# Kernel tuning notes

Hardware: AMD Instinct MI355X
Metric: run time of the kernel (lower is better)

Reference implementation:

```python
import jax, jax.numpy as jnp
import numpy as np

C, T, H = 256, 16, 8
D = C // H  # head dim = 32
SCALE = float((D * T) ** 0.5)


def setup_inputs() -> dict:
    key = jax.random.key(0)
    kx, kk, kq, kv = jax.random.split(key, 4)
    B, P = 8, 1024
    x = jax.random.normal(kx, (B, C, P, T), dtype=jnp.float32)
    # 1x1 conv weights, no bias -> [out_ch, in_ch]
    Wk = jax.random.normal(kk, (C, C), dtype=jnp.float32) * 0.02
    Wq = jax.random.normal(kq, (C, C), dtype=jnp.float32) * 0.02
    Wv = jax.random.normal(kv, (C, C), dtype=jnp.float32) * 0.02
    return {"x": x, "Wk": Wk, "Wq": Wq, "Wv": Wv}


def _proj_split(W, x):
    # 1x1 conv == channel matmul, then split heads: b (h d) p t -> b h d p t
    B, _, P, Tt = x.shape
    y = jnp.einsum('oc,bcpt->bopt', W, x)
    return y.reshape(B, H, D, P, Tt)


def reference(x, Wk, Wq, Wv):
    B, _, P, Tt = x.shape
    k = _proj_split(Wk, x)  # [B,H,D,P,T]
    q = _proj_split(Wq, x)
    v = _proj_split(Wv, x)
    # energy over spatial positions, contracting head-dim and time
    energy = jnp.einsum('bhdpt,bhdqt->bhpq', k, q)  # [B,H,P,P]
    attn = jax.nn.softmax(energy / SCALE, axis=-1)
    out = jnp.einsum('bhpq,bhdpt->bhdqt', attn, v)  # [B,H,D,P,T]
    return out.reshape(B, C, P, Tt)
```

## Files before the change

### kernel.cpp

```cpp
#include <hip/hip_runtime.h>


typedef unsigned short u16;
typedef unsigned int u32;
typedef unsigned long long u64;
typedef __attribute__((ext_vector_type(8))) short bfx8;
typedef __attribute__((ext_vector_type(4))) float fx4;

constexpr float KC1 = 1.4426950408889634f / 22.627416997969522f;

__device__ __forceinline__ u16 f2bf(float f) {
  u32 u = __builtin_bit_cast(u32, f);
  return (u16)((u + 0x7fffu + ((u >> 16) & 1u)) >> 16);
}
__device__ __forceinline__ float bf2f(u16 v) {
  return __builtin_bit_cast(float, (u32)v << 16);
}
__device__ __forceinline__ fx4 mfma16(bfx8 a, bfx8 b, fx4 c) {
  return __builtin_amdgcn_mfma_f32_16x16x32_bf16(a, b, c, 0, 0, 0);
}
typedef __attribute__((address_space(1))) const unsigned int* as1p;
typedef __attribute__((address_space(3))) unsigned int* as3p;
__device__ __forceinline__ void gll16(const void* g, void* l) {
  __builtin_amdgcn_global_load_lds((as1p)g, (as3p)l, 16, 0, 0);
}
#define SB0 __builtin_amdgcn_sched_barrier(0)

template <bool SWAP, int NT, int LK>
__device__ __forceinline__ void gemm1g(const u16* __restrict__ Ag,
                                       const u16* __restrict__ Bg,
                                       u16* lds, fx4 (&acc)[2][4][2][2],
                                       int wv, int lane) {
  const int l15 = lane & 15, kg = lane >> 4, l7 = lane & 7;
  const int wr = wv >> 2, wn = wv & 3;
  const int rsub = lane >> 3, csub = (lane & 7) * 8;
  constexpr int A0 = 0, A1 = 16384, B0 = 32768, B1 = 49152;
  bfx8 af[2][4][2];
  bfx8 bf[2][2][2];

  auto stg = [&](const u16* g, int ldsoff, int tile, int half) {
    const u16* gp = g + (size_t)(half * 128 + wv * 16 + rsub) * LK + tile * 64 + csub;
    u16* lp = lds + ldsoff + half * 8192 + wv * 1024;
    gll16(gp, lp);
    gll16(gp + (size_t)8 * LK, lp + 512);
  };
  auto stgA = [&](int t, int buf) {
    int aoff = buf ? A1 : A0;
    stg(Ag, aoff, t, 0); stg(Ag, aoff, t, 1);
  };
  auto stgB = [&](int t, int buf) {
    int boff = buf ? B1 : B0;
    stg(Bg, boff, t, 0); stg(Bg, boff, t, 1);
  };
  auto LA = [&](int boff, int mh) {
    const u16* base = lds + boff + mh * 8192 + wr * 4096;
#pragma unroll
    for (int mt = 0; mt < 4; ++mt)
#pragma unroll
      for (int kk = 0; kk < 2; ++kk)
        af[mh][mt][kk] = *(const bfx8*)(base + (mt * 16 + l15) * 64 + (((kk << 2) + kg) ^ l7) * 8);
  };
  auto LB = [&](int boff, int nh) {
    const u16* base = lds + boff + nh * 8192 + wn * 2048;
#pragma unroll
    for (int nt = 0; nt < 2; ++nt)
#pragma unroll
      for (int kk = 0; kk < 2; ++kk)
        bf[nh][nt][kk] = *(const bfx8*)(base + (nt * 16 + l15) * 64 + (((kk << 2) + kg) ^ l7) * 8);
  };
  auto MM = [&](int mh, int nh) {
    __builtin_amdgcn_s_setprio(1);
#pragma unroll
    for (int mt = 0; mt < 4; ++mt)
#pragma unroll
      for (int nt = 0; nt < 2; ++nt)
#pragma unroll
        for (int kk = 0; kk < 2; ++kk)
          if constexpr (SWAP)
            acc[mh][mt][nh][nt] = mfma16(bf[nh][nt][kk], af[mh][mt][kk], acc[mh][mt][nh][nt]);
          else
            acc[mh][mt][nh][nt] = mfma16(af[mh][mt][kk], bf[nh][nt][kk], acc[mh][mt][nh][nt]);
    __builtin_amdgcn_s_setprio(0);
  };

  stgA(0, 0); stgB(0, 0);
  stgA(1, 1); stgB(1, 1);
  asm volatile("s_waitcnt vmcnt(8)" ::: "memory");
  __builtin_amdgcn_s_barrier();
  SB0;
  LA(A0, 0);
  LB(B0, 0);

#pragma unroll 1
  for (int t = 0; t < NT - 1; ++t) {
    const int cur = t & 1, nxt = cur ^ 1;
    const int cA = cur ? A1 : A0, cB = cur ? B1 : B0;
    const int nA = cur ? A0 : A1, nB = cur ? B0 : B1;
    LA(cA, 1);
    MM(0, 0);
    LB(cB, 1);
    MM(1, 0);
    asm volatile("s_waitcnt lgkmcnt(0)" ::: "memory");
    asm volatile("s_waitcnt vmcnt(0)" ::: "memory");
    __builtin_amdgcn_s_barrier();
    SB0;
    LB(nB, 0);
    if (t + 2 < NT) stgA(t + 2, cur);
    MM(0, 1);
    LA(nA, 0);
    if (t + 2 < NT) stgB(t + 2, cur);
    MM(1, 1);
  }
  {
    constexpr int cur = (NT - 1) & 1;
    constexpr int cA = cur ? A1 : A0, cB = cur ? B1 : B0;
    LA(cA, 1);
    MM(0, 0);
    LB(cB, 1);
    MM(1, 0);
    MM(0, 1);
    MM(1, 1);
  }
}

__global__ __launch_bounds__(256) void k_wconv(const float* __restrict__ Wk,
                                               const float* __restrict__ Wq,
                                               const float* __restrict__ Wv,
                                               u16* __restrict__ Wall) {
  int blk = blockIdx.x;
  int pr = blk >> 5;
  const float* src = (pr == 0) ? Wk : ((pr == 1) ? Wq : Wv);
  int oc = (blk & 31) * 8 + (threadIdx.x >> 5);
  int Cc = threadIdx.x & 31;
  const float4* s4 = (const float4*)(src + oc * 256 + Cc * 8);
  float4 a = s4[0], b = s4[1];
  alignas(16) u16 t[8] = {f2bf(a.x), f2bf(a.y), f2bf(a.z), f2bf(a.w),
                          f2bf(b.x), f2bf(b.y), f2bf(b.z), f2bf(b.w)};
  int o = pr * 256 + oc;
  int pos = (Cc & ~7) + ((Cc & 7) ^ (o & 7));
  *(uint4*)(Wall + o * 256 + pos * 8) = *(const uint4*)t;
}

__global__ __launch_bounds__(256) void k_xt(const float* __restrict__ x,
                                            u16* __restrict__ Xbf) {
  __shared__ u16 Xs[128 * 256];
  int b = blockIdx.x >> 7;
  int n0 = (blockIdx.x & 127) * 128;
  int tid = threadIdx.x;
  int ng = tid & 31, cgrp = tid >> 5;
  const float* xb = x + (size_t)b * 4194304 + n0 + ng * 4;
#pragma unroll
  for (int it = 0; it < 4; ++it) {
    int Cc = cgrp + it * 8;
    float4 v[8];
#pragma unroll
    for (int i = 0; i < 8; ++i)
      v[i] = *(const float4*)(xb + (size_t)(Cc * 8 + i) * 16384);
#pragma unroll
    for (int j = 0; j < 4; ++j) {
      int n = ng * 4 + j;
      alignas(16) u16 c8v[8];
#pragma unroll
      for (int i = 0; i < 8; ++i) c8v[i] = f2bf(((const float*)&v[i])[j]);
      int pos = (Cc & ~7) + ((Cc & 7) ^ (n & 7));
      *(uint4*)&Xs[n * 256 + pos * 8] = *(const uint4*)c8v;
    }
  }
  __syncthreads();
  u16* xo = Xbf + (size_t)b * 4194304 + (size_t)n0 * 256;
#pragma unroll
  for (int it = 0; it < 16; ++it) {
    int idx = tid + it * 256;
    int n = idx >> 5, chp = idx & 31;
    uint4 v = *(const uint4*)&Xs[n * 256 + chp * 8];
    *(uint4*)&xo[(size_t)n * 256 + chp * 8] = v;
  }
}

__global__ __launch_bounds__(512) void k_proj2(const u16* __restrict__ Xbf,
                                               const u16* __restrict__ Wall,
                                               u16* __restrict__ Kb, u16* __restrict__ Qb,
                                               u16* __restrict__ Vb) {
  __shared__ u16 lds[65536];
  int bid = blockIdx.x;
  int vid = (bid & 7) * 192 + (bid >> 3);
  int nidx = vid / 3;
  int otile = vid - nidx * 3;
  int b = nidx >> 6, ntile = nidx & 63;
  int tid = threadIdx.x, lane = tid & 63, wv = tid >> 6;
  int l15 = lane & 15, kg = lane >> 4;
  int wr = wv >> 2, wn = wv & 3;
  const u16* Ag = Wall + otile * 65536;
  const u16* Bg = Xbf + (size_t)b * 4194304 + (size_t)ntile * 65536;
  fx4 acc[2][4][2][2];
#pragma unroll
  for (int mh = 0; mh < 2; ++mh)
#pragma unroll
    for (int mt = 0; mt < 4; ++mt)
#pragma unroll
      for (int nh = 0; nh < 2; ++nh)
#pragma unroll
        for (int nt = 0; nt < 2; ++nt) acc[mh][mt][nh][nt] = (fx4)0.0f;

  gemm1g<false, 4, 256>(Ag, Bg, lds, acc, wv, lane);

  u16* dst = (otile == 0) ? Kb : ((otile == 1) ? Qb : Vb);
#pragma unroll
  for (int mh = 0; mh < 2; ++mh)
#pragma unroll
    for (int mt = 0; mt < 4; ++mt) {
      int o = mh * 128 + wr * 64 + mt * 16 + kg * 4;
      int h = o >> 5;
      size_t bhro = (size_t)(b * 8 + h) * 524288;
#pragma unroll
      for (int nh = 0; nh < 2; ++nh)
#pragma unroll
        for (int nt = 0; nt < 2; ++nt) {
          int p = ntile * 16 + nh * 8 + wn * 2 + nt;
          size_t ro = bhro + (size_t)p * 512;
          int p7 = p & 7;
#pragma unroll
          for (int j = 0; j < 4; ++j) {
            int f = ((o & 31) + j) * 16 + l15;
            int ch = (f >> 3) ^ p7;
            dst[ro + ch * 8 + (f & 7)] = f2bf(acc[mh][mt][nh][nt][j]);
          }
        }
    }
}

__global__ __launch_bounds__(512) void k_egemm(const u16* __restrict__ Qb,
                                               const u16* __restrict__ Kb,
                                               u16* __restrict__ Pt,
                                               float* __restrict__ Zpart) {
  __shared__ u16 lds[65536];
  int bid = blockIdx.x;
  int vid = (bid & 7) * 128 + (bid >> 3);
  int bh = vid >> 4, qt = (vid >> 2) & 3, pt = vid & 3;
  int q0 = qt * 256, p0 = pt * 256;
  int tid = threadIdx.x, lane = tid & 63, wv = tid >> 6;
  int l15 = lane & 15, kg = lane >> 4;
  int wr = wv >> 2, wn = wv & 3;
  const u16* Ag = Qb + (size_t)bh * 524288 + (size_t)q0 * 512;
  const u16* Bg = Kb + (size_t)bh * 524288 + (size_t)p0 * 512;
  fx4 acc[2][4][2][2];
#pragma unroll
  for (int mh = 0; mh < 2; ++mh)
#pragma unroll
    for (int mt = 0; mt < 4; ++mt)
#pragma unroll
      for (int nh = 0; nh < 2; ++nh)
#pragma unroll
        for (int nt = 0; nt < 2; ++nt) acc[mh][mt][nh][nt] = (fx4)0.0f;

  gemm1g<true, 8, 512>(Ag, Bg, lds, acc, wv, lane);

  size_t pbase = (size_t)bh * 1048576;
  float zac[2][2][4];
#pragma unroll
  for (int nh = 0; nh < 2; ++nh)
#pragma unroll
    for (int nt = 0; nt < 2; ++nt)
#pragma unroll
      for (int j = 0; j < 4; ++j) zac[nh][nt][j] = 0.f;
#pragma unroll
  for (int mh = 0; mh < 2; ++mh)
#pragma unroll
    for (int mt = 0; mt < 4; ++mt) {
      int q = q0 + mh * 128 + wr * 64 + mt * 16 + l15;
      size_t qrow = pbase + (size_t)q * 1024;
      int q7 = l15 & 7;
#pragma unroll
      for (int nh = 0; nh < 2; ++nh)
#pragma unroll
        for (int nt = 0; nt < 2; ++nt) {
          int p4 = p0 + nh * 128 + wn * 32 + nt * 16 + kg * 4;
          alignas(8) u16 e4[4];
#pragma unroll
          for (int j = 0; j < 4; ++j) {
            float e = exp2f(acc[mh][mt][nh][nt][j] * KC1);
            zac[nh][nt][j] += e;
            e4[j] = f2bf(e);
          }
          int ch = (p4 >> 3) ^ q7;
          *(u64*)(Pt + qrow + ch * 8 + (p4 & 7)) = *(const u64*)e4;
        }
    }
#pragma unroll
  for (int nh = 0; nh < 2; ++nh)
#pragma unroll
    for (int nt = 0; nt < 2; ++nt)
#pragma unroll
      for (int j = 0; j < 4; ++j) {
        float v = zac[nh][nt][j];
        v += __shfl_xor(v, 1);
        v += __shfl_xor(v, 2);
        v += __shfl_xor(v, 4);
        v += __shfl_xor(v, 8);
        zac[nh][nt][j] = v;
      }
  if (l15 == 0) {
    size_t zb = (size_t)(qt * 2 + wr) * 65536 + (size_t)bh * 1024;
#pragma unroll
    for (int nh = 0; nh < 2; ++nh)
#pragma unroll
      for (int nt = 0; nt < 2; ++nt) {
        int p4 = p0 + nh * 128 + wn * 32 + nt * 16 + kg * 4;
        float4 zv;
        zv.x = zac[nh][nt][0]; zv.y = zac[nh][nt][1];
        zv.z = zac[nh][nt][2]; zv.w = zac[nh][nt][3];
        *(float4*)&Zpart[zb + p4] = zv;
      }
  }
}

__global__ __launch_bounds__(256) void k_zfinal(const float* __restrict__ Zpart,
                                                float* __restrict__ RZ) {
  int idx = blockIdx.x * 256 + threadIdx.x;
  float s = 0.f;
#pragma unroll
  for (int k = 0; k < 8; ++k) s += Zpart[(size_t)k * 65536 + idx];
  RZ[idx] = 1.0f / s;
}

__global__ __launch_bounds__(256) void k_vt(const u16* __restrict__ Vb,
                                            const float* __restrict__ RZ,
                                            u16* __restrict__ Vt) {
  __shared__ u16 Vl[64 * 512];
  int bh = blockIdx.x >> 4;
  int ptile = blockIdx.x & 15;
  int tid = threadIdx.x;
  const u16* src = Vb + (size_t)bh * 524288 + (size_t)ptile * 32768;
#pragma unroll
  for (int it = 0; it < 16; ++it) {
    int idx = tid + it * 256;
    int pl = idx >> 6, g = idx & 63;
    float rz = RZ[bh * 1024 + ptile * 64 + pl];
    uint4 v = *(const uint4*)&src[(size_t)pl * 512 + g * 8];
    int cf = g ^ (pl & 7);
    u32 w[4] = {v.x, v.y, v.z, v.w};
    alignas(16) u16 c8v[8];
#pragma unroll
    for (int i = 0; i < 4; ++i) {
      c8v[2 * i]     = f2bf(bf2f((u16)w[i]) * rz);
      c8v[2 * i + 1] = f2bf(bf2f((u16)(w[i] >> 16)) * rz);
    }
    *(uint4*)&Vl[pl * 512 + cf * 8] = *(const uint4*)c8v;
  }
  __syncthreads();
  u16* dst = Vt + (size_t)bh * 524288;
#pragma unroll
  for (int it = 0; it < 16; ++it) {
    int f = (tid & 63) + (it & 7) * 64;
    int pc = (tid >> 6) * 2 + (it >> 3);
    int base = pc * 8 * 512 + f;
    u32 x0 = (u32)Vl[base] | ((u32)Vl[base + 512] << 16);
    u32 x1 = (u32)Vl[base + 1024] | ((u32)Vl[base + 1536] << 16);
    u32 x2 = (u32)Vl[base + 2048] | ((u32)Vl[base + 2560] << 16);
    u32 x3 = (u32)Vl[base + 3072] | ((u32)Vl[base + 3584] << 16);
    uint4 pk; pk.x = x0; pk.y = x1; pk.z = x2; pk.w = x3;
    int col = ptile * 8 + (pc ^ (f & 7));
    *(uint4*)&dst[(size_t)f * 1024 + col * 8] = pk;
  }
}

__global__ __launch_bounds__(512) void k_pv(const u16* __restrict__ Pt,
                                            const u16* __restrict__ Vt,
                                            float* __restrict__ out) {
  __shared__ u16 lds[65536];
  int bid = blockIdx.x;
  int vid = (bid & 7) * 64 + (bid >> 3);
  int bh = vid >> 3, tile = vid & 7;
  int q0 = (tile >> 1) * 256, f0 = (tile & 1) * 256;
  int tid = threadIdx.x, lane = tid & 63, wv = tid >> 6;
  int l15 = lane & 15, kg = lane >> 4;
  int wr = wv >> 2, wn = wv & 3;
  const u16* Ag = Pt + (size_t)bh * 1048576 + (size_t)q0 * 1024;
  const u16* Bg = Vt + (size_t)bh * 524288 + (size_t)f0 * 1024;
  fx4 acc[2][4][2][2];
#pragma unroll
  for (int mh = 0; mh < 2; ++mh)
#pragma unroll
    for (int mt = 0; mt < 4; ++mt)
#pragma unroll
      for (int nh = 0; nh < 2; ++nh)
#pragma unroll
        for (int nt = 0; nt < 2; ++nt) acc[mh][mt][nh][nt] = (fx4)0.0f;

  gemm1g<false, 16, 1024>(Ag, Bg, lds, acc, wv, lane);

#pragma unroll
  for (int mh = 0; mh < 2; ++mh)
#pragma unroll
    for (int mt = 0; mt < 4; ++mt) {
      int qb_ = q0 + mh * 128 + wr * 64 + mt * 16 + kg * 4;
#pragma unroll
      for (int nh = 0; nh < 2; ++nh)
#pragma unroll
        for (int nt = 0; nt < 2; ++nt) {
          int f = f0 + nh * 128 + wn * 32 + nt * 16 + l15;
          int d = f >> 4, t = f & 15;
          size_t cb = (size_t)(bh * 32 + d) * 16384 + t;
#pragma unroll
          for (int j = 0; j < 4; ++j)
            out[cb + (size_t)(qb_ + j) * 16] = acc[mh][mt][nh][nt][j];
        }
    }
}

extern "C" void kernel_launch(void* const* d_in, const int* in_sizes, int n_in,
                              void* d_out, int out_size, void* d_ws, size_t ws_size,
                              hipStream_t stream) {
  (void)in_sizes; (void)n_in; (void)out_size; (void)ws_size;
  const float* x  = (const float*)d_in[0];
  const float* Wk = (const float*)d_in[1];
  const float* Wq = (const float*)d_in[2];
  const float* Wv = (const float*)d_in[3];
  float* out = (float*)d_out;

  u16* Kb  = (u16*)d_ws;
  u16* Qb  = Kb + 33554432;
  u16* Vb  = Qb + 33554432;
  u16* Xbf = Vb + 33554432;
  u16* Pt  = Xbf;
  u16* Vt  = Qb;
  float* Zpart = (float*)(Kb + 167772160);
  float* RZ = Zpart + 524288;
  u16* Wall = (u16*)(RZ + 65536);

  k_wconv<<<96, 256, 0, stream>>>(Wk, Wq, Wv, Wall);
  k_xt<<<1024, 256, 0, stream>>>(x, Xbf);
  k_proj2<<<1536, 512, 0, stream>>>(Xbf, Wall, Kb, Qb, Vb);
  k_egemm<<<1024, 512, 0, stream>>>(Qb, Kb, Pt, Zpart);
  k_zfinal<<<256, 256, 0, stream>>>(Zpart, RZ);
  k_vt<<<1024, 256, 0, stream>>>(Vb, RZ, Vt);
  k_pv<<<512, 512, 0, stream>>>(Pt, Vt, out);
}
```

Baseline: 361.2 us.

## Restructure shared GEMM into 8-phase pipeline and vectorize epilogue stores

The shared bf16 MFMA GEMM routine is rewritten as an eight-phase ping-pong schedule that interleaves half-tile global-to-LDS loads with quarter-block MFMA groups, separated by barriers and partial vmcnt waits. This hides load latency at finer granularity and cuts register use for A fragments. The projection and PV kernels now use the swapped operand order, so each lane holds consecutive output elements, letting the epilogues emit 8-byte bf16 and 16-byte float4 stores instead of scalar ones. The cost is many more barriers per K step and tricky buffer-reuse ordering.

```diff
diff --git a/kernel.cpp b/kernel.cpp
--- a/kernel.cpp
+++ b/kernel.cpp
@@ -24,19 +24,26 @@
 __device__ __forceinline__ void gll16(const void* g, void* l) {
   __builtin_amdgcn_global_load_lds((as1p)g, (as3p)l, 16, 0, 0);
 }
-#define SB0 __builtin_amdgcn_sched_barrier(0)
+__device__ __forceinline__ void midbar_() { __builtin_amdgcn_s_barrier(); }
+__device__ __forceinline__ void pend_() {
+  __builtin_amdgcn_s_barrier();
+  __builtin_amdgcn_sched_barrier(0);
+}
+#define VMC4 do { asm volatile("s_waitcnt vmcnt(4)" ::: "memory"); \
+                  __builtin_amdgcn_sched_barrier(0); } while (0)
+#define VMC0 do { asm volatile("s_waitcnt vmcnt(0)" ::: "memory"); \
+                  __builtin_amdgcn_sched_barrier(0); } while (0)
 
 template <bool SWAP, int NT, int LK>
-__device__ __forceinline__ void gemm1g(const u16* __restrict__ Ag,
-                                       const u16* __restrict__ Bg,
-                                       u16* lds, fx4 (&acc)[2][4][2][2],
-                                       int wv, int lane) {
+__device__ __forceinline__ void gemm8(const u16* __restrict__ Ag,
+                                      const u16* __restrict__ Bg,
+                                      u16* lds, fx4 (&acc)[2][4][2][2],
+                                      int wv, int lane) {
   const int l15 = lane & 15, kg = lane >> 4, l7 = lane & 7;
   const int wr = wv >> 2, wn = wv & 3;
   const int rsub = lane >> 3, csub = (lane & 7) * 8;
   constexpr int A0 = 0, A1 = 16384, B0 = 32768, B1 = 49152;
-  bfx8 af[2][4][2];
-  bfx8 bf[2][2][2];
+  bfx8 af[4][2], bf[2][2][2];
 
   auto stg = [&](const u16* g, int ldsoff, int tile, int half) {
     const u16* gp = g + (size_t)(half * 128 + wv * 16 + rsub) * LK + tile * 64 + csub;
@@ -44,21 +51,13 @@
     gll16(gp, lp);
     gll16(gp + (size_t)8 * LK, lp + 512);
   };
-  auto stgA = [&](int t, int buf) {
-    int aoff = buf ? A1 : A0;
-    stg(Ag, aoff, t, 0); stg(Ag, aoff, t, 1);
-  };
-  auto stgB = [&](int t, int buf) {
-    int boff = buf ? B1 : B0;
-    stg(Bg, boff, t, 0); stg(Bg, boff, t, 1);
-  };
   auto LA = [&](int boff, int mh) {
     const u16* base = lds + boff + mh * 8192 + wr * 4096;
 #pragma unroll
     for (int mt = 0; mt < 4; ++mt)
 #pragma unroll
       for (int kk = 0; kk < 2; ++kk)
-        af[mh][mt][kk] = *(const bfx8*)(base + (mt * 16 + l15) * 64 + (((kk << 2) + kg) ^ l7) * 8);
+        af[mt][kk] = *(const bfx8*)(base + (mt * 16 + l15) * 64 + (((kk << 2) + kg) ^ l7) * 8);
   };
   auto LB = [&](int boff, int nh) {
     const u16* base = lds + boff + nh * 8192 + wn * 2048;
@@ -75,51 +74,52 @@
 #pragma unroll
       for (int nt = 0; nt < 2; ++nt)
 #pragma unroll
-        for (int kk = 0; kk < 2; ++kk)
+        for (int kk = 0; kk < 2; ++kk) {
           if constexpr (SWAP)
-            acc[mh][mt][nh][nt] = mfma16(bf[nh][nt][kk], af[mh][mt][kk], acc[mh][mt][nh][nt]);
+            acc[mh][mt][nh][nt] = mfma16(bf[nh][nt][kk], af[mt][kk], acc[mh][mt][nh][nt]);
           else
-            acc[mh][mt][nh][nt] = mfma16(af[mh][mt][kk], bf[nh][nt][kk], acc[mh][mt][nh][nt]);
+            acc[mh][mt][nh][nt] = mfma16(af[mt][kk], bf[nh][nt][kk], acc[mh][mt][nh][nt]);
+        }
     __builtin_amdgcn_s_setprio(0);
   };
 
-  stgA(0, 0); stgB(0, 0);
-  stgA(1, 1); stgB(1, 1);
-  asm volatile("s_waitcnt vmcnt(8)" ::: "memory");
-  __builtin_amdgcn_s_barrier();
-  SB0;
-  LA(A0, 0);
-  LB(B0, 0);
-
+  stg(Ag, A0, 0, 0); stg(Ag, A0, 0, 1);
+  stg(Bg, B0, 0, 0); stg(Bg, B0, 0, 1);
+  stg(Ag, A1, 1, 0); stg(Bg, B1, 1, 1);
+  VMC4;
+  pend_();
+
+  constexpr int NI = NT / 2;
 #pragma unroll 1
-  for (int t = 0; t < NT - 1; ++t) {
-    const int cur = t & 1, nxt = cur ^ 1;
-    const int cA = cur ? A1 : A0, cB = cur ? B1 : B0;
-    const int nA = cur ? A0 : A1, nB = cur ? B0 : B1;
-    LA(cA, 1);
-    MM(0, 0);
-    LB(cB, 1);
-    MM(1, 0);
-    asm volatile("s_waitcnt lgkmcnt(0)" ::: "memory");
-    asm volatile("s_waitcnt vmcnt(0)" ::: "memory");
-    __builtin_amdgcn_s_barrier();
-    SB0;
-    LB(nB, 0);
-    if (t + 2 < NT) stgA(t + 2, cur);
-    MM(0, 1);
-    LA(nA, 0);
-    if (t + 2 < NT) stgB(t + 2, cur);
-    MM(1, 1);
-  }
-  {
-    constexpr int cur = (NT - 1) & 1;
-    constexpr int cA = cur ? A1 : A0, cB = cur ? B1 : B0;
-    LA(cA, 1);
-    MM(0, 0);
-    LB(cB, 1);
-    MM(1, 0);
-    MM(0, 1);
-    MM(1, 1);
+  for (int i = 0; i < NI; ++i) {
+    const int t = 2 * i;
+    const bool more = (i + 1 < NI);
+    LA(A0, 0); LB(B0, 0);
+    stg(Ag, A1, t + 1, 1);
+    midbar_(); MM(0, 0); pend_();
+    LB(B0, 1);
+    stg(Bg, B1, t + 1, 0);
+    midbar_(); MM(0, 1); pend_();
+    LA(A0, 1);
+    if (more) stg(Ag, A0, t + 2, 0);
+    midbar_(); MM(1, 1); pend_();
+    if (more) stg(Bg, B0, t + 2, 1);
+    midbar_(); MM(1, 0);
+    if (more) { VMC4; } else { VMC0; }
+    pend_();
+    LA(A1, 0); LB(B1, 0);
+    if (more) stg(Ag, A0, t + 2, 1);
+    midbar_(); MM(0, 0); pend_();
+    LB(B1, 1);
+    if (more) stg(Bg, B0, t + 2, 0);
+    midbar_(); MM(0, 1); pend_();
+    LA(A1, 1);
+    if (more) stg(Ag, A1, t + 3, 0);
+    midbar_(); MM(1, 1); pend_();
+    if (more) stg(Bg, B1, t + 3, 1);
+    midbar_(); MM(1, 0);
+    if (more) { VMC4; }
+    pend_();
   }
 }
 
@@ -202,29 +202,30 @@
 #pragma unroll
         for (int nt = 0; nt < 2; ++nt) acc[mh][mt][nh][nt] = (fx4)0.0f;
 
-  gemm1g<false, 4, 256>(Ag, Bg, lds, acc, wv, lane);
+  gemm8<true, 4, 256>(Ag, Bg, lds, acc, wv, lane);
 
   u16* dst = (otile == 0) ? Kb : ((otile == 1) ? Qb : Vb);
 #pragma unroll
   for (int mh = 0; mh < 2; ++mh)
 #pragma unroll
     for (int mt = 0; mt < 4; ++mt) {
-      int o = mh * 128 + wr * 64 + mt * 16 + kg * 4;
+      int o = mh * 128 + wr * 64 + mt * 16 + l15;
       int h = o >> 5;
+      int d = o & 31;
       size_t bhro = (size_t)(b * 8 + h) * 524288;
+      int f0 = d * 16 + kg * 4;
+      int f7 = f0 & 7;
+      int fc = f0 >> 3;
 #pragma unroll
       for (int nh = 0; nh < 2; ++nh)
 #pragma unroll
         for (int nt = 0; nt < 2; ++nt) {
           int p = ntile * 16 + nh * 8 + wn * 2 + nt;
-          size_t ro = bhro + (size_t)p * 512;
-          int p7 = p & 7;
-#pragma unroll
-          for (int j = 0; j < 4; ++j) {
-            int f = ((o & 31) + j) * 16 + l15;
-            int ch = (f >> 3) ^ p7;
-            dst[ro + ch * 8 + (f & 7)] = f2bf(acc[mh][mt][nh][nt][j]);
-          }
+          alignas(8) u16 e4[4];
+#pragma unroll
+          for (int j = 0; j < 4; ++j) e4[j] = f2bf(acc[mh][mt][nh][nt][j]);
+          int ch = fc ^ (p & 7);
+          *(u64*)(dst + bhro + (size_t)p * 512 + ch * 8 + f7) = *(const u64*)e4;
         }
     }
 }
@@ -253,7 +254,7 @@
 #pragma unroll
         for (int nt = 0; nt < 2; ++nt) acc[mh][mt][nh][nt] = (fx4)0.0f;
 
-  gemm1g<true, 8, 512>(Ag, Bg, lds, acc, wv, lane);
+  gemm8<true, 8, 512>(Ag, Bg, lds, acc, wv, lane);
 
   size_t pbase = (size_t)bh * 1048576;
   float zac[2][2][4];
@@ -387,23 +388,25 @@
 #pragma unroll
         for (int nt = 0; nt < 2; ++nt) acc[mh][mt][nh][nt] = (fx4)0.0f;
 
-  gemm1g<false, 16, 1024>(Ag, Bg, lds, acc, wv, lane);
+  gemm8<true, 16, 1024>(Ag, Bg, lds, acc, wv, lane);
 
 #pragma unroll
   for (int mh = 0; mh < 2; ++mh)
 #pragma unroll
     for (int mt = 0; mt < 4; ++mt) {
-      int qb_ = q0 + mh * 128 + wr * 64 + mt * 16 + kg * 4;
+      int q = q0 + mh * 128 + wr * 64 + mt * 16 + l15;
 #pragma unroll
       for (int nh = 0; nh < 2; ++nh)
 #pragma unroll
         for (int nt = 0; nt < 2; ++nt) {
-          int f = f0 + nh * 128 + wn * 32 + nt * 16 + l15;
-          int d = f >> 4, t = f & 15;
-          size_t cb = (size_t)(bh * 32 + d) * 16384 + t;
-#pragma unroll
-          for (int j = 0; j < 4; ++j)
-            out[cb + (size_t)(qb_ + j) * 16] = acc[mh][mt][nh][nt][j];
+          int fb = f0 + nh * 128 + wn * 32 + nt * 16 + kg * 4;
+          int d = fb >> 4, t0 = fb & 15;
+          float4 v;
+          v.x = acc[mh][mt][nh][nt][0];
+          v.y = acc[mh][mt][nh][nt][1];
+          v.z = acc[mh][mt][nh][nt][2];
+          v.w = acc[mh][mt][nh][nt][3];
+          *(float4*)&out[(size_t)(bh * 32 + d) * 16384 + (size_t)q * 16 + t0] = v;
         }
     }
 }
```

Result: faster. 348.4 us (-3.5%).
